# Kernel optimization log

Hardware: AMD Instinct MI355X
Metric: run time of the kernel (lower is better)

The kernel has to match this reference:

```python
import jax, jax.numpy as jnp
import numpy as np

SPLINE_ORDER = 3
BN_EPS = 1e-5


def make_grid(grid_size, lo=-1.0, hi=1.0):
    # torch KANLinear grid: uniform on [lo,hi] extended by spline_order knots each side
    h = (hi - lo) / grid_size
    return jnp.arange(-SPLINE_ORDER, grid_size + SPLINE_ORDER + 1, dtype=jnp.float32) * h + lo


def b_splines(x, grid, k=SPLINE_ORDER):
    # x: [...], grid: [G+2k+1] -> bases [..., G+k] (Cox-de Boor recursion)
    x = x[..., None]
    bases = ((x >= grid[:-1]) & (x < grid[1:])).astype(x.dtype)
    for j in range(1, k + 1):
        left = (x - grid[: -(j + 1)]) / (grid[j:-1] - grid[: -(j + 1)])
        right = (grid[j + 1:] - x) / (grid[j + 1:] - grid[1:-j])
        bases = left * bases[..., :-1] + right * bases[..., 1:]
    return bases


def extract_patches(x, d):
    # 3x3 dilated sliding windows, stride 1, padding == dilation -> same HxW
    B, C, H, W = x.shape
    xp = jnp.pad(x, ((0, 0), (0, 0), (d, d), (d, d)))
    pats = [xp[:, :, ki * d:ki * d + H, kj * d:kj * d + W]
            for ki in range(3) for kj in range(3)]
    return jnp.stack(pats, axis=-1)  # [B,C,H,W,9] (kh-major, matching torch Unfold)


def batchnorm(x, g, b):
    # training-mode BN (torch default forward): batch statistics, biased variance
    mean = x.mean(axis=(0, 2, 3), keepdims=True)
    var = x.var(axis=(0, 2, 3), keepdims=True)
    return (x - mean) / jnp.sqrt(var + BN_EPS) * g[None, :, None, None] + b[None, :, None, None]


def se_block(x, w1, w2):
    y = x.mean(axis=(2, 3))                                  # [B,C]
    y = jax.nn.sigmoid(jax.nn.relu(y @ w1.T) @ w2.T)         # [B,C]
    return x * y[:, :, None, None]


def kan_conv(x, base_w, spline_w, grid, dilation):
    # one KANLinear(9->1) per (out,in) channel pair, summed over in channels
    p = extract_patches(x, dilation)                          # [B,Ci,H,W,9]
    base = jnp.einsum('bihwk,oik->bohw', jax.nn.silu(p), base_w)
    bs = b_splines(p, grid)                                   # [B,Ci,H,W,9,G+k]
    spl = jnp.einsum('bihwkg,oikg->bohw', bs, spline_w)
    return base + spl


def kan_branch(x, base_w, spline_w, grid, dilation, bn_g, bn_b, se_w1, se_w2):
    y = kan_conv(x, base_w, spline_w, grid, dilation)
    y = jax.nn.relu(batchnorm(y, bn_g, bn_b))
    return se_block(y, se_w1, se_w2)


def setup_inputs() -> dict:
    key = jax.random.key(0)
    ks = jax.random.split(key, 16)
    B, Ci, Co, H, W = 2, 64, 64, 64, 64
    r = Co // 16
    d = {"x": jax.random.normal(ks[0], (B, Ci, H, W), jnp.float32)}
    for i, (bname, G) in enumerate([(6, 3), (12, 6), (18, 9)]):
        kk = jax.random.split(ks[1 + i], 4)
        d[f"base_w{bname}"] = jax.random.normal(kk[0], (Co, Ci, 9), jnp.float32) / np.sqrt(9.0 * Ci)
        d[f"spline_w{bname}"] = jax.random.normal(kk[1], (Co, Ci, 9, G + SPLINE_ORDER), jnp.float32) * (0.1 / np.sqrt(9.0 * Ci))
        d[f"bn{bname}_g"] = jnp.ones((Co,), jnp.float32)
        d[f"bn{bname}_b"] = jnp.zeros((Co,), jnp.float32)
        d[f"se{bname}_w1"] = jax.random.normal(kk[2], (r, Co), jnp.float32) / np.sqrt(Co)
        d[f"se{bname}_w2"] = jax.random.normal(kk[3], (Co, r), jnp.float32) / np.sqrt(r)
    d["gp_conv_w"] = jax.random.normal(ks[4], (Co, Ci), jnp.float32) / np.sqrt(Ci)
    d["gp_conv_b"] = jnp.zeros((Co,), jnp.float32)
    d["gp_bn_g"] = jnp.ones((Co,), jnp.float32)
    d["gp_bn_b"] = jnp.zeros((Co,), jnp.float32)
    d["gp_se_w1"] = jax.random.normal(ks[5], (r, Co), jnp.float32) / np.sqrt(Co)
    d["gp_se_w2"] = jax.random.normal(ks[6], (Co, r), jnp.float32) / np.sqrt(r)
    d["fuse_w"] = jax.random.normal(ks[7], (Co, 4 * Co), jnp.float32) / np.sqrt(4.0 * Co)
    d["fuse_b"] = jnp.zeros((Co,), jnp.float32)
    d["fuse_bn_g"] = jnp.ones((Co,), jnp.float32)
    d["fuse_bn_b"] = jnp.zeros((Co,), jnp.float32)
    return d


def reference(x, base_w6, spline_w6, bn6_g, bn6_b, se6_w1, se6_w2,
              base_w12, spline_w12, bn12_g, bn12_b, se12_w1, se12_w2,
              base_w18, spline_w18, bn18_g, bn18_b, se18_w1, se18_w2,
              gp_conv_w, gp_conv_b, gp_bn_g, gp_bn_b, gp_se_w1, gp_se_w2,
              fuse_w, fuse_b, fuse_bn_g, fuse_bn_b):
    B, Ci, H, W = x.shape
    # global-pool branch: avgpool -> 1x1 conv -> BN -> ReLU -> SE -> bilinear
    # upsample (1x1 source => pure broadcast, align_corners irrelevant)
    gp = x.mean(axis=(2, 3)) @ gp_conv_w.T + gp_conv_b      # [B,Co]
    gp = gp[:, :, None, None]
    gp = jax.nn.relu(batchnorm(gp, gp_bn_g, gp_bn_b))
    gp = se_block(gp, gp_se_w1, gp_se_w2)
    gp = jnp.broadcast_to(gp, (B, gp.shape[1], H, W))
    # KAN dilated branches
    b6 = kan_branch(x, base_w6, spline_w6, make_grid(3), 6, bn6_g, bn6_b, se6_w1, se6_w2)
    b12 = kan_branch(x, base_w12, spline_w12, make_grid(6), 12, bn12_g, bn12_b, se12_w1, se12_w2)
    b18 = kan_branch(x, base_w18, spline_w18, make_grid(9), 18, bn18_g, bn18_b, se18_w1, se18_w2)
    cat = jnp.concatenate([b6, b12, b18, gp], axis=1)        # [B,4Co,H,W]
    out = jnp.einsum('bihw,oi->bohw', cat, fuse_w) + fuse_b[None, :, None, None]
    out = jax.nn.relu(batchnorm(out, fuse_bn_g, fuse_bn_b))
    return out
```

## Files before the change

kernel.cpp:

```cpp
#include <hip/hip_runtime.h>
#include <hip/hip_bf16.h>
#include <math.h>

#define DEV __device__ __forceinline__

static constexpr int HW  = 4096;
static constexpr int POS = 8192;
static constexpr int SLAB = 6 * 64 * 4096;

typedef __attribute__((ext_vector_type(8)))  short short8;
typedef __attribute__((ext_vector_type(16))) float floatx16;

template<int G>
DEV void bsplines(float x, float* out ) {
  const float h = 2.0f / (float)G;
  float knot[G + 7];
#pragma unroll
  for (int t = 0; t < G + 7; ++t) knot[t] = -1.0f + (float)(t - 3) * h;
  float bb[G + 6];
#pragma unroll
  for (int t = 0; t < G + 6; ++t) bb[t] = (x >= knot[t] && x < knot[t + 1]) ? 1.0f : 0.0f;
#pragma unroll
  for (int j = 1; j <= 3; ++j) {
    const float inv = (float)G / (2.0f * (float)j);
#pragma unroll
    for (int t = 0; t < G + 6 - j; ++t) {
      float left  = (x - knot[t]) * inv;
      float right = (knot[t + j + 1] - x) * inv;
      bb[t] = left * bb[t] + right * bb[t + 1];
    }
  }
#pragma unroll
  for (int t = 0; t < G + 3; ++t) out[t] = bb[t];
}

DEV float sigmoidf_(float x) { return 1.0f / (1.0f + __expf(-x)); }

DEV float block_reduce_256(float v, float* sb) {
  __syncthreads();
#pragma unroll
  for (int off = 32; off > 0; off >>= 1) v += __shfl_down(v, off, 64);
  int lane = threadIdx.x & 63, wid = threadIdx.x >> 6;
  if (lane == 0) sb[wid] = v;
  __syncthreads();
  return sb[0] + sb[1] + sb[2] + sb[3];
}


template<int CF>
DEV void wprep_body(const float* __restrict__ base_w, const float* __restrict__ spline_w,
                    __hip_bfloat16* __restrict__ Wt, int bid) {
  constexpr int KC = 64 * CF;
  int lin = bid * 256 + threadIdx.x;
  int ic = lin % KC;
  int rest = lin / KC;
  int o = rest & 63, tap = rest >> 6;
  int c = ic % CF, i = ic / CF;
  float v = (c == 0) ? base_w[(o * 64 + i) * 9 + tap]
                     : spline_w[((o * 64 + i) * 9 + tap) * (CF - 1) + (c - 1)];
  Wt[lin] = __float2bfloat16(v);
}

template<int G>
DEV void c0r_body(int ki, const float* __restrict__ sw, float* __restrict__ out,
                  float* shmem ) {
  constexpr int NB = G + 3;
  int o = threadIdx.x & 63, part = threadIdx.x >> 6;
  float b0[NB];
  bsplines<G>(0.0f, b0);
  float s = 0.0f;
  for (int kj = 0; kj < 3; ++kj) {
    int tap = ki * 3 + kj;
    for (int i = part * 16; i < part * 16 + 16; ++i) {
      const float* p = sw + ((size_t)(o * 64 + i) * 9 + tap) * NB;
#pragma unroll
      for (int c = 0; c < NB; ++c) s += p[c] * b0[c];
    }
  }
  shmem[part * 64 + o] = s;
  __syncthreads();
  if (part == 0)
    out[ki * 64 + o] = shmem[o] + shmem[64 + o] + shmem[128 + o] + shmem[192 + o];
}

__global__ void prep_k(const float* bw0, const float* sw0, const float* bw1, const float* sw1,
                       const float* bw2, const float* sw2,
                       __hip_bfloat16* W0, __hip_bfloat16* W1, __hip_bfloat16* W2,
                       float* C0r, const float* fuse_w, float* fwT,
                       const float* x, float* xm, float* accz ) {
  __shared__ float shmem[256];
  int bid = blockIdx.x, tid = threadIdx.x;
  if (bid < 1008)      { wprep_body<7>(bw0, sw0, W0, bid); }
  else if (bid < 2448) { wprep_body<10>(bw1, sw1, W1, bid - 1008); }
  else if (bid < 4320) { wprep_body<13>(bw2, sw2, W2, bid - 2448); }
  else if (bid < 4329) {
    int idx = bid - 4320, br = idx / 3, ki = idx % 3;
    if (br == 0)      c0r_body<3>(ki, sw0, C0r, shmem);
    else if (br == 1) c0r_body<6>(ki, sw1, C0r + 192, shmem);
    else              c0r_body<9>(ki, sw2, C0r + 384, shmem);
  } else if (bid < 4377) {
    int lin = (bid - 4329) * 256 + tid;
    int o = lin & 63, i2 = lin >> 6;
    fwT[i2 * 64 + o] = fuse_w[o * 256 + i2];
  } else if (bid < 4505) {
    int bi = bid - 4377;
    const float* p = x + (size_t)bi * HW;
    float s = 0.0f;
    for (int t = tid; t < HW; t += 256) s += p[t];
    s = block_reduce_256(s, shmem);
    if (tid == 0) xm[bi] = s * (1.0f / HW);
  } else {
    for (int t = tid; t < 896; t += 256) accz[t] = 0.0f;
  }
}

template<int G, int D>
DEV void features_body(const float* __restrict__ x, __hip_bfloat16* __restrict__ F, int bid,
                       __hip_bfloat16* lds ) {
  constexpr int CF = G + 4;
  constexpr int NB = G + 3;
  constexpr int WP = 64 + 2 * D;
  constexpr int NG = WP / 4;
  constexpr int KC = 64 * CF;
  int i = threadIdx.x & 63, ws = threadIdx.x >> 6;
  int wpg = bid % NG;
  int rest = bid / NG;
  int h = rest & 63, b = rest >> 6;
  int wp = wpg * 4 + ws;
  int w = wp - D;
  float xv = (w >= 0 && w < 64) ? x[((size_t)(b * 64 + i) * 64 + h) * 64 + w] : 0.0f;
  float s = xv * sigmoidf_(xv);
  float bas[NB];
  bsplines<G>(xv, bas);
  __hip_bfloat16* dst = lds + (ws * 64 + i) * CF;
  dst[0] = __float2bfloat16(s);
#pragma unroll
  for (int c = 1; c < CF; ++c) dst[c] = __float2bfloat16(bas[c - 1]);
  __syncthreads();
  constexpr int TOT2 = 4 * 64 * CF / 2;
  uint* g = (uint*)(F + ((size_t)((b * 64 + h) * WP) + wpg * 4) * KC);
  const uint* l = (const uint*)lds;
  for (int t = threadIdx.x; t < TOT2; t += 256) g[t] = l[t];
}

__global__ void features_all_k(const float* __restrict__ x, __hip_bfloat16* F0,
                               __hip_bfloat16* F1, __hip_bfloat16* F2) {
  __shared__ __hip_bfloat16 lds[4 * 64 * 13];
  int bid = blockIdx.x;
  if (bid < 2432)      features_body<3, 6>(x, F0, bid, lds);
  else if (bid < 5248) features_body<6, 12>(x, F1, bid - 2432, lds);
  else                 features_body<9, 18>(x, F2, bid - 5248, lds);
}

DEV floatx16 mfma_bf16(short8 a, short8 b, floatx16 c) {
  return __builtin_amdgcn_mfma_f32_32x32x16_bf16(a, b, c, 0, 0, 0);
}

template<int CF, int DD>
DEV void conv_dev(int ki, int b, int hp, const short* __restrict__ F,
                  const short* __restrict__ W, const float* __restrict__ C0r,
                  float* __restrict__ ypart, int br) {
  constexpr int KC = 64 * CF;
  constexpr int WP = 64 + 2 * DD;
  int wv = threadIdx.x >> 6;
  int lane = threadIdx.x & 63;
  int lr = lane & 31, lq = lane >> 5;
  int hs = hp * 2 + wv;
  int h_out = hs - (ki - 1) * DD;
  bool valid = (h_out >= 0 && h_out < 64);
  int h_tgt = valid ? h_out : (h_out < 0 ? h_out + 64 : h_out - 64);
  float* yb = ypart + (size_t)ki * SLAB + ((size_t)((br * 2 + b) * 64 + h_tgt)) * 4096;

  if (!valid) {
    const float* c0 = C0r + (br * 3 + ki) * 64;
#pragma unroll
    for (int wh = 0; wh < 2; ++wh) {
      int w = wh * 32 + lr;
#pragma unroll
      for (int ot = 0; ot < 2; ++ot)
#pragma unroll
        for (int reg = 0; reg < 16; ++reg) {
          int o = (reg & 3) + 8 * (reg >> 2) + 4 * lq + 32 * ot;
          yb[(size_t)o * 64 + w] = c0[o];
        }
    }
    return;
  }

  floatx16 acc[2][2];
#pragma unroll
  for (int ot = 0; ot < 2; ++ot)
#pragma unroll
    for (int wh = 0; wh < 2; ++wh)
#pragma unroll
      for (int r = 0; r < 16; ++r) acc[ot][wh][r] = 0.0f;

  const short* rowF = F + (size_t)(b * 64 + hs) * WP * KC;
  const short* wb = W + (size_t)(ki * 3) * 64 * KC + lr * KC + lq * 8;
  const short* fb = rowF + lr * KC + lq * 8;
#pragma unroll
  for (int kj = 0; kj < 3; ++kj) {
    const short* w0p = wb + kj * (64 * KC);
    const short* f0p = fb + kj * (DD * KC);
#pragma unroll 4
    for (int s = 0; s < 4 * CF; ++s) {
      short8 a0 = *(const short8*)(w0p + s * 16);
      short8 a1 = *(const short8*)(w0p + 32 * KC + s * 16);
      short8 b0 = *(const short8*)(f0p + s * 16);
      short8 b1 = *(const short8*)(f0p + 32 * KC + s * 16);
      acc[0][0] = mfma_bf16(a0, b0, acc[0][0]);
      acc[0][1] = mfma_bf16(a0, b1, acc[0][1]);
      acc[1][0] = mfma_bf16(a1, b0, acc[1][0]);
      acc[1][1] = mfma_bf16(a1, b1, acc[1][1]);
    }
  }

#pragma unroll
  for (int ot = 0; ot < 2; ++ot)
#pragma unroll
    for (int wh = 0; wh < 2; ++wh) {
      int w = wh * 32 + lr;
#pragma unroll
      for (int reg = 0; reg < 16; ++reg) {
        int o = (reg & 3) + 8 * (reg >> 2) + 4 * lq + 32 * ot;
        yb[(size_t)o * 64 + w] = acc[ot][wh][reg];
      }
    }
}

__global__ __launch_bounds__(128) void conv_all_k(
    const short* __restrict__ F0, const short* __restrict__ F1, const short* __restrict__ F2,
    const short* __restrict__ W0, const short* __restrict__ W1, const short* __restrict__ W2,
    const float* __restrict__ C0r, float* __restrict__ ypart) {
  int bid = blockIdx.x;
  int e  = bid & 7;
  int t  = bid >> 3;
  int ki = t % 3;
  int m  = (t / 3) * 8 + e;
  int br = m >> 6, b = (m >> 5) & 1, hp = m & 31;
  if (br == 0)      conv_dev<7, 6>(ki, b, hp, F0, W0, C0r, ypart, 0);
  else if (br == 1) conv_dev<10, 12>(ki, b, hp, F1, W1, C0r, ypart, 1);
  else              conv_dev<13, 18>(ki, b, hp, F2, W2, C0r, ypart, 2);
}

__global__ void rb_k(float* __restrict__ yp, float* __restrict__ bnacc_s,
                     float* __restrict__ bnacc_q) {
  int bid = blockIdx.x;
  int bb = bid / 256, chunk = bid % 256;
  int br = bb >> 1;
  int tid = threadIdx.x;
  size_t base = (size_t)bb * 262144 + chunk * 1024 + tid * 4;
  float4 v = *(const float4*)(yp + base);
#pragma unroll
  for (int s2 = 1; s2 < 3; ++s2) {
    float4 u = *(const float4*)(yp + base + (size_t)s2 * SLAB);
    v.x += u.x; v.y += u.y; v.z += u.z; v.w += u.w;
  }
  *(float4*)(yp + base) = v;
  float s = v.x + v.y + v.z + v.w;
  float q = v.x * v.x + v.y * v.y + v.z * v.z + v.w * v.w;
  s += __shfl_down(s, 8, 16); s += __shfl_down(s, 4, 16);
  s += __shfl_down(s, 2, 16); s += __shfl_down(s, 1, 16);
  q += __shfl_down(q, 8, 16); q += __shfl_down(q, 4, 16);
  q += __shfl_down(q, 2, 16); q += __shfl_down(q, 1, 16);
  if ((tid & 15) == 0) {
    int o = (chunk * 16 + (tid >> 4)) & 63;
    atomicAdd(&bnacc_s[br * 64 + o], s);
    atomicAdd(&bnacc_q[br * 64 + o], q);
  }
}

__global__ void sesum_k(const float* __restrict__ y, const float* __restrict__ bnacc_s,
                        const float* __restrict__ bnacc_q,
                        const float* g0, const float* b0p, const float* g1, const float* b1p,
                        const float* g2, const float* b2p, float* __restrict__ se_acc) {
  int bid = blockIdx.x;
  int bb = bid >> 6, h = bid & 63;
  int br = bb >> 1;
  int tid = threadIdx.x;
  int o = tid >> 2, wq = tid & 3;
  const float* gptr = (br == 0) ? g0 : ((br == 1) ? g1 : g2);
  const float* bptr = (br == 0) ? b0p : ((br == 1) ? b1p : b2p);
  float mu = bnacc_s[br * 64 + o] * (1.0f / POS);
  float var = bnacc_q[br * 64 + o] * (1.0f / POS) - mu * mu;
  float kk = gptr[o] / sqrtf(var + 1e-5f);
  float cc = bptr[o] - mu * kk;
  const float* row = y + (size_t)bb * 262144 + (size_t)h * 4096 + o * 64 + wq * 16;
  float s = 0.0f;
#pragma unroll
  for (int j = 0; j < 4; ++j) {
    float4 v = *(const float4*)(row + j * 4);
    float a;
    a = v.x * kk + cc; s += (a > 0.0f) ? a : 0.0f;
    a = v.y * kk + cc; s += (a > 0.0f) ? a : 0.0f;
    a = v.z * kk + cc; s += (a > 0.0f) ? a : 0.0f;
    a = v.w * kk + cc; s += (a > 0.0f) ? a : 0.0f;
  }
  s += __shfl_down(s, 2, 4);
  s += __shfl_down(s, 1, 4);
  if (wq == 0) atomicAdd(&se_acc[bb * 64 + o], s);
}

__global__ void semlp_gp_k(const float* __restrict__ se_acc,
                           const float* __restrict__ bnacc_s, const float* __restrict__ bnacc_q,
                           const float* g0, const float* b0p, const float* g1, const float* b1p,
                           const float* g2, const float* b2p,
                           const float* w10, const float* w11, const float* w12,
                           const float* w20, const float* w21, const float* w22,
                           float* __restrict__ A1, float* __restrict__ A0,
                           const float* __restrict__ xm, const float* __restrict__ gw,
                           const float* __restrict__ gb, const float* __restrict__ bng,
                           const float* __restrict__ bnb, const float* __restrict__ gpw1,
                           const float* __restrict__ gpw2, const float* __restrict__ fuse_w,
                           float* __restrict__ fuse_gp) {
  __shared__ float sm[64];
  __shared__ float g0s[2][64], gp1s[2][64], gpvs[2][64];
  int tid = threadIdx.x;
  if (blockIdx.x < 6) {
    int bb = blockIdx.x, br = bb >> 1;
    const float* w1 = (br == 0) ? w10 : ((br == 1) ? w11 : w12);
    const float* w2 = (br == 0) ? w20 : ((br == 1) ? w21 : w22);
    const float* gptr = (br == 0) ? g0 : ((br == 1) ? g1 : g2);
    const float* bptr = (br == 0) ? b0p : ((br == 1) ? b1p : b2p);
    if (tid < 64) sm[tid] = se_acc[bb * 64 + tid] * (1.0f / HW);
    __syncthreads();
    if (tid < 64) {
      int o = tid;
      float z[4];
#pragma unroll
      for (int j = 0; j < 4; ++j) {
        float s = 0.0f;
        for (int c2 = 0; c2 < 64; ++c2) s += sm[c2] * w1[j * 64 + c2];
        z[j] = (s > 0.0f) ? s : 0.0f;
      }
      float t = 0.0f;
#pragma unroll
      for (int j = 0; j < 4; ++j) t += z[j] * w2[o * 4 + j];
      t = sigmoidf_(t);
      float mu = bnacc_s[br * 64 + o] * (1.0f / POS);
      float var = bnacc_q[br * 64 + o] * (1.0f / POS) - mu * mu;
      float kk = gptr[o] / sqrtf(var + 1e-5f);
      float cc = bptr[o] - mu * kk;
      A1[bb * 64 + o] = kk * t;
      A0[bb * 64 + o] = cc * t;
    }
  } else {
    int b = tid >> 6, o = tid & 63;
    float gv = gb[o];
    for (int i = 0; i < 64; ++i) gv += xm[b * 64 + i] * gw[o * 64 + i];
    g0s[b][o] = gv;
    __syncthreads();
    float mu = 0.5f * (g0s[0][o] + g0s[1][o]);
    float df = g0s[0][o] - g0s[1][o];
    float var = 0.25f * df * df;
    float v = (gv - mu) / sqrtf(var + 1e-5f) * bng[o] + bnb[o];
    v = (v > 0.0f) ? v : 0.0f;
    gp1s[b][o] = v;
    __syncthreads();
    float z[4];
#pragma unroll
    for (int j = 0; j < 4; ++j) {
      float s = 0.0f;
      for (int c2 = 0; c2 < 64; ++c2) s += gp1s[b][c2] * gpw1[j * 64 + c2];
      z[j] = (s > 0.0f) ? s : 0.0f;
    }
    float t = 0.0f;
#pragma unroll
    for (int j = 0; j < 4; ++j) t += z[j] * gpw2[o * 4 + j];
    t = sigmoidf_(t);
    gpvs[b][o] = v * t;
    __syncthreads();
    float fg = 0.0f;
    for (int c2 = 0; c2 < 64; ++c2) fg += fuse_w[o * 256 + 192 + c2] * gpvs[b][c2];
    fuse_gp[b * 64 + o] = fg;
  }
}

__global__ __launch_bounds__(256) void fuse_k(
    const float* __restrict__ y, const float* __restrict__ A1, const float* __restrict__ A0,
    const float* __restrict__ fwT, const float* __restrict__ fb, const float* __restrict__ fgp,
    float* __restrict__ tmp, float* __restrict__ fstat) {
  int bid = blockIdx.x;
  int b = bid >> 7, h = (bid >> 1) & 63, wh = bid & 1;
  int tid = threadIdx.x;
  int wg = tid & 7, og = tid >> 3;
  int w0 = wg * 4, o0 = og * 2;
  float acc[2][4] = {};
  __shared__ float As[64][32];
  __shared__ float Ws[64][64];
  for (int br = 0; br < 3; ++br) {
#pragma unroll
    for (int m = 0; m < 8; ++m) {
      int lin = tid + m * 256;
      int oc = lin >> 5, wl = lin & 31;
      float v = y[(size_t)(br * 2 + b) * 262144 + (size_t)h * 4096 + oc * 64 + wh * 32 + wl];
      float a1 = A1[(br * 2 + b) * 64 + oc], a0 = A0[(br * 2 + b) * 64 + oc];
      v = v * a1 + a0;
      As[oc][wl] = (v > 0.0f) ? v : 0.0f;
    }
#pragma unroll
    for (int m = 0; m < 16; ++m) {
      int lin = tid + m * 256;
      int oc = lin >> 6, ol = lin & 63;
      Ws[oc][ol] = fwT[(br * 64 + oc) * 64 + ol];
    }
    __syncthreads();
#pragma unroll 8
    for (int ict = 0; ict < 64; ++ict) {
      float4 a = *reinterpret_cast<const float4*>(&As[ict][w0]);
      float2 wv = *reinterpret_cast<const float2*>(&Ws[ict][o0]);
      acc[0][0] += wv.x * a.x; acc[0][1] += wv.x * a.y; acc[0][2] += wv.x * a.z; acc[0][3] += wv.x * a.w;
      acc[1][0] += wv.y * a.x; acc[1][1] += wv.y * a.y; acc[1][2] += wv.y * a.z; acc[1][3] += wv.y * a.w;
    }
    __syncthreads();
  }
  float* tp = tmp + (size_t)(b * 64 + h) * 4096 + wh * 32;
  float ps[2], pq[2];
#pragma unroll
  for (int oo = 0; oo < 2; ++oo) {
    int o = o0 + oo;
    float bias = fb[o] + fgp[b * 64 + o];
    float4 v = make_float4(acc[oo][0] + bias, acc[oo][1] + bias,
                           acc[oo][2] + bias, acc[oo][3] + bias);
    *reinterpret_cast<float4*>(&tp[o * 64 + w0]) = v;
    ps[oo] = v.x + v.y + v.z + v.w;
    pq[oo] = v.x * v.x + v.y * v.y + v.z * v.z + v.w * v.w;
  }
  __syncthreads();
#pragma unroll
  for (int oo = 0; oo < 2; ++oo) { As[o0 + oo][wg] = ps[oo]; Ws[o0 + oo][wg] = pq[oo]; }
  __syncthreads();
  if (tid < 64) {
    float s = 0.0f, q = 0.0f;
#pragma unroll
    for (int r = 0; r < 8; ++r) { s += As[tid][r]; q += Ws[tid][r]; }
    atomicAdd(&fstat[tid], s);
    atomicAdd(&fstat[64 + tid], q);
  }
}

__global__ void final_k(const float* __restrict__ tmp, const float* __restrict__ fstat,
                        const float* __restrict__ g, const float* __restrict__ bb,
                        float* __restrict__ out) {
  int lin = blockIdx.x * 256 + threadIdx.x;
  int w = lin & 63, h2 = (lin >> 6) & 63, o = (lin >> 12) & 63, b = lin >> 18;
  float v = tmp[((size_t)(b * 64 + h2) * 64 + o) * 64 + w];
  float m = fstat[o] * (1.0f / POS);
  float var = fstat[64 + o] * (1.0f / POS) - m * m;
  float kk = g[o] / sqrtf(var + 1e-5f);
  float r = (v - m) * kk + bb[o];
  out[lin] = (r > 0.0f) ? r : 0.0f;
}

extern "C" void kernel_launch(void* const* d_in, const int* in_sizes, int n_in,
                              void* d_out, int out_size, void* d_ws, size_t ws_size,
                              hipStream_t stream) {
  const float* x = (const float*)d_in[0];
  const float* base_w[3]   = {(const float*)d_in[1],  (const float*)d_in[7],  (const float*)d_in[13]};
  const float* spline_w[3] = {(const float*)d_in[2],  (const float*)d_in[8],  (const float*)d_in[14]};
  const float* bn_g[3]     = {(const float*)d_in[3],  (const float*)d_in[9],  (const float*)d_in[15]};
  const float* bn_b[3]     = {(const float*)d_in[4],  (const float*)d_in[10], (const float*)d_in[16]};
  const float* se_w1[3]    = {(const float*)d_in[5],  (const float*)d_in[11], (const float*)d_in[17]};
  const float* se_w2[3]    = {(const float*)d_in[6],  (const float*)d_in[12], (const float*)d_in[18]};
  const float* gp_conv_w = (const float*)d_in[19];
  const float* gp_conv_b = (const float*)d_in[20];
  const float* gp_bn_g   = (const float*)d_in[21];
  const float* gp_bn_b   = (const float*)d_in[22];
  const float* gp_se_w1  = (const float*)d_in[23];
  const float* gp_se_w2  = (const float*)d_in[24];
  const float* fuse_w    = (const float*)d_in[25];
  const float* fuse_b    = (const float*)d_in[26];
  const float* fuse_bn_g = (const float*)d_in[27];
  const float* fuse_bn_b = (const float*)d_in[28];
  float* out = (float*)d_out;

  char* wsp = (char*)d_ws;
  auto alloc = [&](size_t bytes) -> char* {
    char* p = wsp;
    wsp += (bytes + 255) & ~(size_t)255;
    return p;
  };
  __hip_bfloat16* F0 = (__hip_bfloat16*)alloc((size_t)2 * 64 * 76 * 448 * 2);
  __hip_bfloat16* F1 = (__hip_bfloat16*)alloc((size_t)2 * 64 * 88 * 640 * 2);
  __hip_bfloat16* F2 = (__hip_bfloat16*)alloc((size_t)2 * 64 * 100 * 832 * 2);
  __hip_bfloat16* W0 = (__hip_bfloat16*)alloc((size_t)9 * 64 * 448 * 2);
  __hip_bfloat16* W1 = (__hip_bfloat16*)alloc((size_t)9 * 64 * 640 * 2);
  __hip_bfloat16* W2 = (__hip_bfloat16*)alloc((size_t)9 * 64 * 832 * 2);
  float* C0r   = (float*)alloc((size_t)3 * 3 * 64 * 4);
  float* ypart = (float*)alloc((size_t)3 * SLAB * 4);
  float* y     = ypart;
  float* tmp   = ypart + SLAB;
  float* A1  = (float*)alloc(384 * 4);
  float* A0  = (float*)alloc(384 * 4);
  float* xm  = (float*)alloc(128 * 4);
  float* fgp = (float*)alloc(128 * 4);
  float* fwT = (float*)alloc((size_t)12288 * 4);
  float* accz = (float*)alloc(896 * 4);
  float* fstat   = accz;
  float* bnacc_s = accz + 128;
  float* bnacc_q = accz + 320;
  float* se_acc  = accz + 512;

  prep_k<<<4506, 256, 0, stream>>>(base_w[0], spline_w[0], base_w[1], spline_w[1],
                                   base_w[2], spline_w[2], W0, W1, W2, C0r,
                                   fuse_w, fwT, x, xm, accz);
  features_all_k<<<8448, 256, 0, stream>>>(x, F0, F1, F2);
  conv_all_k<<<576, 128, 0, stream>>>(
      (const short*)F0, (const short*)F1, (const short*)F2,
      (const short*)W0, (const short*)W1, (const short*)W2, C0r, ypart);
  rb_k<<<1536, 256, 0, stream>>>(ypart, bnacc_s, bnacc_q);
  sesum_k<<<384, 256, 0, stream>>>(y, bnacc_s, bnacc_q, bn_g[0], bn_b[0], bn_g[1], bn_b[1],
                                   bn_g[2], bn_b[2], se_acc);
  semlp_gp_k<<<7, 128, 0, stream>>>(se_acc, bnacc_s, bnacc_q, bn_g[0], bn_b[0], bn_g[1], bn_b[1],
                                    bn_g[2], bn_b[2], se_w1[0], se_w1[1], se_w1[2],
                                    se_w2[0], se_w2[1], se_w2[2], A1, A0,
                                    xm, gp_conv_w, gp_conv_b, gp_bn_g, gp_bn_b,
                                    gp_se_w1, gp_se_w2, fuse_w, fgp);
  fuse_k<<<256, 256, 0, stream>>>(y, A1, A0, fwT, fuse_b, fgp, tmp, fstat);
  final_k<<<2048, 256, 0, stream>>>(tmp, fstat, fuse_bn_g, fuse_bn_b, out);
}
```

Before: 296.3 us.

## Merge prep with features, fuse BN/SE reductions, and fold SE MLP into fuse kernel

Combines the weight-prep and feature-expansion kernels into one launch, replaces the separate split-K reduce, BN-stat, and SE-sum kernels with a single per-channel kernel that sums the partials and computes both statistics without atomics, and recomputes the SE MLP and global-pool branch redundantly inside every fuse block. The aim is to cut launch count and inter-kernel gaps. In exchange, the new reduction kernel runs only 192 blocks, each striding through memory at 256-byte steps with poor coalescing. Every fuse block also repeats a small serial MLP.

```diff
diff --git a/kernel.cpp b/kernel.cpp
--- a/kernel.cpp
+++ b/kernel.cpp
@@ -81,37 +81,6 @@
   __syncthreads();
   if (part == 0)
     out[ki * 64 + o] = shmem[o] + shmem[64 + o] + shmem[128 + o] + shmem[192 + o];
-}
-
-__global__ void prep_k(const float* bw0, const float* sw0, const float* bw1, const float* sw1,
-                       const float* bw2, const float* sw2,
-                       __hip_bfloat16* W0, __hip_bfloat16* W1, __hip_bfloat16* W2,
-                       float* C0r, const float* fuse_w, float* fwT,
-                       const float* x, float* xm, float* accz ) {
-  __shared__ float shmem[256];
-  int bid = blockIdx.x, tid = threadIdx.x;
-  if (bid < 1008)      { wprep_body<7>(bw0, sw0, W0, bid); }
-  else if (bid < 2448) { wprep_body<10>(bw1, sw1, W1, bid - 1008); }
-  else if (bid < 4320) { wprep_body<13>(bw2, sw2, W2, bid - 2448); }
-  else if (bid < 4329) {
-    int idx = bid - 4320, br = idx / 3, ki = idx % 3;
-    if (br == 0)      c0r_body<3>(ki, sw0, C0r, shmem);
-    else if (br == 1) c0r_body<6>(ki, sw1, C0r + 192, shmem);
-    else              c0r_body<9>(ki, sw2, C0r + 384, shmem);
-  } else if (bid < 4377) {
-    int lin = (bid - 4329) * 256 + tid;
-    int o = lin & 63, i2 = lin >> 6;
-    fwT[i2 * 64 + o] = fuse_w[o * 256 + i2];
-  } else if (bid < 4505) {
-    int bi = bid - 4377;
-    const float* p = x + (size_t)bi * HW;
-    float s = 0.0f;
-    for (int t = tid; t < HW; t += 256) s += p[t];
-    s = block_reduce_256(s, shmem);
-    if (tid == 0) xm[bi] = s * (1.0f / HW);
-  } else {
-    for (int t = tid; t < 896; t += 256) accz[t] = 0.0f;
-  }
 }
 
 template<int G, int D>
@@ -143,13 +112,42 @@
   for (int t = threadIdx.x; t < TOT2; t += 256) g[t] = l[t];
 }
 
-__global__ void features_all_k(const float* __restrict__ x, __hip_bfloat16* F0,
-                               __hip_bfloat16* F1, __hip_bfloat16* F2) {
+__global__ void prepfeat_k(const float* __restrict__ x,
+                           __hip_bfloat16* F0, __hip_bfloat16* F1, __hip_bfloat16* F2,
+                           const float* bw0, const float* sw0, const float* bw1,
+                           const float* sw1, const float* bw2, const float* sw2,
+                           __hip_bfloat16* W0, __hip_bfloat16* W1, __hip_bfloat16* W2,
+                           float* C0r, const float* fuse_w, float* fwT,
+                           float* xm, float* accz ) {
   __shared__ __hip_bfloat16 lds[4 * 64 * 13];
-  int bid = blockIdx.x;
-  if (bid < 2432)      features_body<3, 6>(x, F0, bid, lds);
-  else if (bid < 5248) features_body<6, 12>(x, F1, bid - 2432, lds);
-  else                 features_body<9, 18>(x, F2, bid - 5248, lds);
+  __shared__ float shmem[256];
+  int bid = blockIdx.x, tid = threadIdx.x;
+  if (bid < 2432)      { features_body<3, 6>(x, F0, bid, lds); return; }
+  else if (bid < 5248) { features_body<6, 12>(x, F1, bid - 2432, lds); return; }
+  else if (bid < 8448) { features_body<9, 18>(x, F2, bid - 5248, lds); return; }
+  int pb = bid - 8448;
+  if (pb < 1008)      { wprep_body<7>(bw0, sw0, W0, pb); }
+  else if (pb < 2448) { wprep_body<10>(bw1, sw1, W1, pb - 1008); }
+  else if (pb < 4320) { wprep_body<13>(bw2, sw2, W2, pb - 2448); }
+  else if (pb < 4329) {
+    int idx = pb - 4320, br = idx / 3, ki = idx % 3;
+    if (br == 0)      c0r_body<3>(ki, sw0, C0r, shmem);
+    else if (br == 1) c0r_body<6>(ki, sw1, C0r + 192, shmem);
+    else              c0r_body<9>(ki, sw2, C0r + 384, shmem);
+  } else if (pb < 4377) {
+    int lin = (pb - 4329) * 256 + tid;
+    int o = lin & 63, i2 = lin >> 6;
+    fwT[i2 * 64 + o] = fuse_w[o * 256 + i2];
+  } else if (pb < 4505) {
+    int bi = pb - 4377;
+    const float* p = x + (size_t)bi * HW;
+    float s = 0.0f;
+    for (int t = tid; t < HW; t += 256) s += p[t];
+    s = block_reduce_256(s, shmem);
+    if (tid == 0) xm[bi] = s * (1.0f / HW);
+  } else {
+    for (int t = tid; t < 896; t += 256) accz[t] = 0.0f;
+  }
 }
 
 DEV floatx16 mfma_bf16(short8 a, short8 b, floatx16 c) {
@@ -243,94 +241,88 @@
   else              conv_dev<13, 18>(ki, b, hp, F2, W2, C0r, ypart, 2);
 }
 
-__global__ void rb_k(float* __restrict__ yp, float* __restrict__ bnacc_s,
-                     float* __restrict__ bnacc_q) {
-  int bid = blockIdx.x;
-  int bb = bid / 256, chunk = bid % 256;
-  int br = bb >> 1;
-  int tid = threadIdx.x;
-  size_t base = (size_t)bb * 262144 + chunk * 1024 + tid * 4;
-  float4 v = *(const float4*)(yp + base);
-#pragma unroll
-  for (int s2 = 1; s2 < 3; ++s2) {
-    float4 u = *(const float4*)(yp + base + (size_t)s2 * SLAB);
-    v.x += u.x; v.y += u.y; v.z += u.z; v.w += u.w;
-  }
-  *(float4*)(yp + base) = v;
-  float s = v.x + v.y + v.z + v.w;
-  float q = v.x * v.x + v.y * v.y + v.z * v.z + v.w * v.w;
-  s += __shfl_down(s, 8, 16); s += __shfl_down(s, 4, 16);
-  s += __shfl_down(s, 2, 16); s += __shfl_down(s, 1, 16);
-  q += __shfl_down(q, 8, 16); q += __shfl_down(q, 4, 16);
-  q += __shfl_down(q, 2, 16); q += __shfl_down(q, 1, 16);
-  if ((tid & 15) == 0) {
-    int o = (chunk * 16 + (tid >> 4)) & 63;
-    atomicAdd(&bnacc_s[br * 64 + o], s);
-    atomicAdd(&bnacc_q[br * 64 + o], q);
-  }
-}
-
-__global__ void sesum_k(const float* __restrict__ y, const float* __restrict__ bnacc_s,
-                        const float* __restrict__ bnacc_q,
-                        const float* g0, const float* b0p, const float* g1, const float* b1p,
-                        const float* g2, const float* b2p, float* __restrict__ se_acc) {
-  int bid = blockIdx.x;
-  int bb = bid >> 6, h = bid & 63;
-  int br = bb >> 1;
-  int tid = threadIdx.x;
-  int o = tid >> 2, wq = tid & 3;
+__global__ void bnsesum_k(float* __restrict__ yp, float* __restrict__ bnacc_s,
+                          float* __restrict__ bnacc_q,
+                          const float* g0, const float* b0p, const float* g1, const float* b1p,
+                          const float* g2, const float* b2p, float* __restrict__ se_acc) {
+  int br = blockIdx.x >> 6, o = blockIdx.x & 63;
+  __shared__ float sb[4];
+  float s = 0.0f, q = 0.0f;
+  for (int idx = threadIdx.x; idx < POS; idx += 256) {
+    int b = idx >> 12, rem = idx & 4095;
+    int h = rem >> 6, w = rem & 63;
+    size_t base = ((size_t)((br * 2 + b) * 64 + h)) * 4096 + o * 64 + w;
+    float v = yp[base] + yp[base + SLAB] + yp[base + 2 * (size_t)SLAB];
+    yp[base] = v;
+    s += v; q += v * v;
+  }
+  s = block_reduce_256(s, sb);
+  q = block_reduce_256(q, sb);
+  if (threadIdx.x == 0) { bnacc_s[br * 64 + o] = s; bnacc_q[br * 64 + o] = q; }
+  float m = s * (1.0f / POS);
+  float var = q * (1.0f / POS) - m * m;
   const float* gptr = (br == 0) ? g0 : ((br == 1) ? g1 : g2);
   const float* bptr = (br == 0) ? b0p : ((br == 1) ? b1p : b2p);
-  float mu = bnacc_s[br * 64 + o] * (1.0f / POS);
-  float var = bnacc_q[br * 64 + o] * (1.0f / POS) - mu * mu;
   float kk = gptr[o] / sqrtf(var + 1e-5f);
-  float cc = bptr[o] - mu * kk;
-  const float* row = y + (size_t)bb * 262144 + (size_t)h * 4096 + o * 64 + wq * 16;
-  float s = 0.0f;
-#pragma unroll
-  for (int j = 0; j < 4; ++j) {
-    float4 v = *(const float4*)(row + j * 4);
-    float a;
-    a = v.x * kk + cc; s += (a > 0.0f) ? a : 0.0f;
-    a = v.y * kk + cc; s += (a > 0.0f) ? a : 0.0f;
-    a = v.z * kk + cc; s += (a > 0.0f) ? a : 0.0f;
-    a = v.w * kk + cc; s += (a > 0.0f) ? a : 0.0f;
-  }
-  s += __shfl_down(s, 2, 4);
-  s += __shfl_down(s, 1, 4);
-  if (wq == 0) atomicAdd(&se_acc[bb * 64 + o], s);
-}
-
-__global__ void semlp_gp_k(const float* __restrict__ se_acc,
-                           const float* __restrict__ bnacc_s, const float* __restrict__ bnacc_q,
-                           const float* g0, const float* b0p, const float* g1, const float* b1p,
-                           const float* g2, const float* b2p,
-                           const float* w10, const float* w11, const float* w12,
-                           const float* w20, const float* w21, const float* w22,
-                           float* __restrict__ A1, float* __restrict__ A0,
-                           const float* __restrict__ xm, const float* __restrict__ gw,
-                           const float* __restrict__ gb, const float* __restrict__ bng,
-                           const float* __restrict__ bnb, const float* __restrict__ gpw1,
-                           const float* __restrict__ gpw2, const float* __restrict__ fuse_w,
-                           float* __restrict__ fuse_gp) {
-  __shared__ float sm[64];
-  __shared__ float g0s[2][64], gp1s[2][64], gpvs[2][64];
+  float cc = bptr[o] - m * kk;
+  float s0 = 0.0f, s1 = 0.0f;
+  for (int idx = threadIdx.x; idx < POS; idx += 256) {
+    int b = idx >> 12, rem = idx & 4095;
+    int h = rem >> 6, w = rem & 63;
+    float a = yp[((size_t)((br * 2 + b) * 64 + h)) * 4096 + o * 64 + w] * kk + cc;
+    a = (a > 0.0f) ? a : 0.0f;
+    if (b == 0) s0 += a; else s1 += a;
+  }
+  s0 = block_reduce_256(s0, sb);
+  s1 = block_reduce_256(s1, sb);
+  if (threadIdx.x == 0) {
+    se_acc[(br * 2 + 0) * 64 + o] = s0;
+    se_acc[(br * 2 + 1) * 64 + o] = s1;
+  }
+}
+
+__global__ __launch_bounds__(256) void fuse_k(
+    const float* __restrict__ y, const float* __restrict__ se_acc,
+    const float* __restrict__ bnacc_s, const float* __restrict__ bnacc_q,
+    const float* g0, const float* b0p, const float* g1, const float* b1p,
+    const float* g2, const float* b2p,
+    const float* w10, const float* w11, const float* w12,
+    const float* w20, const float* w21, const float* w22,
+    const float* __restrict__ xm, const float* __restrict__ gw,
+    const float* __restrict__ gb, const float* __restrict__ bng,
+    const float* __restrict__ bnb, const float* __restrict__ gpw1,
+    const float* __restrict__ gpw2, const float* __restrict__ fuse_w,
+    const float* __restrict__ fwT, const float* __restrict__ fb,
+    float* __restrict__ tmp, float* __restrict__ fstat) {
+  __shared__ float As[64][32];
+  __shared__ float Ws[64][64];
+  __shared__ float sem[384], A1l[384], A0l[384], fgpl[128], gsc[384];
+  int bid = blockIdx.x;
+  int b = bid >> 7, h = (bid >> 1) & 63, wh = bid & 1;
   int tid = threadIdx.x;
-  if (blockIdx.x < 6) {
-    int bb = blockIdx.x, br = bb >> 1;
-    const float* w1 = (br == 0) ? w10 : ((br == 1) ? w11 : w12);
-    const float* w2 = (br == 0) ? w20 : ((br == 1) ? w21 : w22);
-    const float* gptr = (br == 0) ? g0 : ((br == 1) ? g1 : g2);
-    const float* bptr = (br == 0) ? b0p : ((br == 1) ? b1p : b2p);
-    if (tid < 64) sm[tid] = se_acc[bb * 64 + tid] * (1.0f / HW);
-    __syncthreads();
-    if (tid < 64) {
-      int o = tid;
+
+  for (int u = tid; u < 384; u += 256) sem[u] = se_acc[u] * (1.0f / HW);
+  __syncthreads();
+  if (tid < 128) {
+    int bgp = tid >> 6, o = tid & 63;
+    float gv = gb[o];
+    for (int i = 0; i < 64; ++i) gv += xm[bgp * 64 + i] * gw[o * 64 + i];
+    gsc[tid] = gv;
+  }
+  if (tid < 64) {
+    int o = tid;
+#pragma unroll
+    for (int bb = 0; bb < 6; ++bb) {
+      int br = bb >> 1;
+      const float* w1 = (br == 0) ? w10 : ((br == 1) ? w11 : w12);
+      const float* w2 = (br == 0) ? w20 : ((br == 1) ? w21 : w22);
+      const float* g_ = (br == 0) ? g0 : ((br == 1) ? g1 : g2);
+      const float* b_ = (br == 0) ? b0p : ((br == 1) ? b1p : b2p);
       float z[4];
 #pragma unroll
       for (int j = 0; j < 4; ++j) {
         float s = 0.0f;
-        for (int c2 = 0; c2 < 64; ++c2) s += sm[c2] * w1[j * 64 + c2];
+        for (int c2 = 0; c2 < 64; ++c2) s += sem[bb * 64 + c2] * w1[j * 64 + c2];
         z[j] = (s > 0.0f) ? s : 0.0f;
       }
       float t = 0.0f;
@@ -339,63 +331,57 @@
       t = sigmoidf_(t);
       float mu = bnacc_s[br * 64 + o] * (1.0f / POS);
       float var = bnacc_q[br * 64 + o] * (1.0f / POS) - mu * mu;
-      float kk = gptr[o] / sqrtf(var + 1e-5f);
-      float cc = bptr[o] - mu * kk;
-      A1[bb * 64 + o] = kk * t;
-      A0[bb * 64 + o] = cc * t;
-    }
-  } else {
-    int b = tid >> 6, o = tid & 63;
-    float gv = gb[o];
-    for (int i = 0; i < 64; ++i) gv += xm[b * 64 + i] * gw[o * 64 + i];
-    g0s[b][o] = gv;
-    __syncthreads();
-    float mu = 0.5f * (g0s[0][o] + g0s[1][o]);
-    float df = g0s[0][o] - g0s[1][o];
+      float kk = g_[o] / sqrtf(var + 1e-5f);
+      float cc = b_[o] - mu * kk;
+      A1l[bb * 64 + o] = kk * t;
+      A0l[bb * 64 + o] = cc * t;
+    }
+  }
+  __syncthreads();
+  if (tid < 128) {
+    int o = tid & 63;
+    float mu = 0.5f * (gsc[o] + gsc[64 + o]);
+    float df = gsc[o] - gsc[64 + o];
     float var = 0.25f * df * df;
-    float v = (gv - mu) / sqrtf(var + 1e-5f) * bng[o] + bnb[o];
-    v = (v > 0.0f) ? v : 0.0f;
-    gp1s[b][o] = v;
-    __syncthreads();
+    float v = (gsc[tid] - mu) / sqrtf(var + 1e-5f) * bng[o] + bnb[o];
+    gsc[128 + tid] = (v > 0.0f) ? v : 0.0f;
+  }
+  __syncthreads();
+  if (tid < 128) {
+    int bgp = tid >> 6, o = tid & 63;
     float z[4];
 #pragma unroll
     for (int j = 0; j < 4; ++j) {
       float s = 0.0f;
-      for (int c2 = 0; c2 < 64; ++c2) s += gp1s[b][c2] * gpw1[j * 64 + c2];
+      for (int c2 = 0; c2 < 64; ++c2) s += gsc[128 + bgp * 64 + c2] * gpw1[j * 64 + c2];
       z[j] = (s > 0.0f) ? s : 0.0f;
     }
     float t = 0.0f;
 #pragma unroll
     for (int j = 0; j < 4; ++j) t += z[j] * gpw2[o * 4 + j];
     t = sigmoidf_(t);
-    gpvs[b][o] = v * t;
-    __syncthreads();
+    gsc[256 + tid] = gsc[128 + tid] * t;
+  }
+  __syncthreads();
+  if (tid < 128) {
+    int bgp = tid >> 6, o = tid & 63;
     float fg = 0.0f;
-    for (int c2 = 0; c2 < 64; ++c2) fg += fuse_w[o * 256 + 192 + c2] * gpvs[b][c2];
-    fuse_gp[b * 64 + o] = fg;
-  }
-}
-
-__global__ __launch_bounds__(256) void fuse_k(
-    const float* __restrict__ y, const float* __restrict__ A1, const float* __restrict__ A0,
-    const float* __restrict__ fwT, const float* __restrict__ fb, const float* __restrict__ fgp,
-    float* __restrict__ tmp, float* __restrict__ fstat) {
-  int bid = blockIdx.x;
-  int b = bid >> 7, h = (bid >> 1) & 63, wh = bid & 1;
-  int tid = threadIdx.x;
+    for (int c2 = 0; c2 < 64; ++c2) fg += fuse_w[o * 256 + 192 + c2] * gsc[256 + bgp * 64 + c2];
+    fgpl[tid] = fg;
+  }
+  __syncthreads();
+
   int wg = tid & 7, og = tid >> 3;
   int w0 = wg * 4, o0 = og * 2;
   float acc[2][4] = {};
-  __shared__ float As[64][32];
-  __shared__ float Ws[64][64];
   for (int br = 0; br < 3; ++br) {
 #pragma unroll
     for (int m = 0; m < 8; ++m) {
       int lin = tid + m * 256;
       int oc = lin >> 5, wl = lin & 31;
       float v = y[(size_t)(br * 2 + b) * 262144 + (size_t)h * 4096 + oc * 64 + wh * 32 + wl];
-      float a1 = A1[(br * 2 + b) * 64 + oc], a0 = A0[(br * 2 + b) * 64 + oc];
-      v = v * a1 + a0;
+      int idx = (br * 2 + b) * 64 + oc;
+      v = v * A1l[idx] + A0l[idx];
       As[oc][wl] = (v > 0.0f) ? v : 0.0f;
     }
 #pragma unroll
@@ -419,7 +405,7 @@
 #pragma unroll
   for (int oo = 0; oo < 2; ++oo) {
     int o = o0 + oo;
-    float bias = fb[o] + fgp[b * 64 + o];
+    float bias = fb[o] + fgpl[b * 64 + o];
     float4 v = make_float4(acc[oo][0] + bias, acc[oo][1] + bias,
                            acc[oo][2] + bias, acc[oo][3] + bias);
     *reinterpret_cast<float4*>(&tp[o * 64 + w0]) = v;
@@ -490,10 +476,7 @@
   float* ypart = (float*)alloc((size_t)3 * SLAB * 4);
   float* y     = ypart;
   float* tmp   = ypart + SLAB;
-  float* A1  = (float*)alloc(384 * 4);
-  float* A0  = (float*)alloc(384 * 4);
   float* xm  = (float*)alloc(128 * 4);
-  float* fgp = (float*)alloc(128 * 4);
   float* fwT = (float*)alloc((size_t)12288 * 4);
   float* accz = (float*)alloc(896 * 4);
   float* fstat   = accz;
@@ -501,21 +484,19 @@
   float* bnacc_q = accz + 320;
   float* se_acc  = accz + 512;
 
-  prep_k<<<4506, 256, 0, stream>>>(base_w[0], spline_w[0], base_w[1], spline_w[1],
-                                   base_w[2], spline_w[2], W0, W1, W2, C0r,
-                                   fuse_w, fwT, x, xm, accz);
-  features_all_k<<<8448, 256, 0, stream>>>(x, F0, F1, F2);
+  prepfeat_k<<<12954, 256, 0, stream>>>(x, F0, F1, F2,
+                                        base_w[0], spline_w[0], base_w[1], spline_w[1],
+                                        base_w[2], spline_w[2], W0, W1, W2, C0r,
+                                        fuse_w, fwT, xm, accz);
   conv_all_k<<<576, 128, 0, stream>>>(
       (const short*)F0, (const short*)F1, (const short*)F2,
       (const short*)W0, (const short*)W1, (const short*)W2, C0r, ypart);
-  rb_k<<<1536, 256, 0, stream>>>(ypart, bnacc_s, bnacc_q);
-  sesum_k<<<384, 256, 0, stream>>>(y, bnacc_s, bnacc_q, bn_g[0], bn_b[0], bn_g[1], bn_b[1],
-                                   bn_g[2], bn_b[2], se_acc);
-  semlp_gp_k<<<7, 128, 0, stream>>>(se_acc, bnacc_s, bnacc_q, bn_g[0], bn_b[0], bn_g[1], bn_b[1],
-                                    bn_g[2], bn_b[2], se_w1[0], se_w1[1], se_w1[2],
-                                    se_w2[0], se_w2[1], se_w2[2], A1, A0,
-                                    xm, gp_conv_w, gp_conv_b, gp_bn_g, gp_bn_b,
-                                    gp_se_w1, gp_se_w2, fuse_w, fgp);
-  fuse_k<<<256, 256, 0, stream>>>(y, A1, A0, fwT, fuse_b, fgp, tmp, fstat);
+  bnsesum_k<<<192, 256, 0, stream>>>(ypart, bnacc_s, bnacc_q, bn_g[0], bn_b[0],
+                                     bn_g[1], bn_b[1], bn_g[2], bn_b[2], se_acc);
+  fuse_k<<<256, 256, 0, stream>>>(y, se_acc, bnacc_s, bnacc_q,
+                                  bn_g[0], bn_b[0], bn_g[1], bn_b[1], bn_g[2], bn_b[2],
+                                  se_w1[0], se_w1[1], se_w1[2], se_w2[0], se_w2[1], se_w2[2],
+                                  xm, gp_conv_w, gp_conv_b, gp_bn_g, gp_bn_b,
+                                  gp_se_w1, gp_se_w2, fuse_w, fwT, fuse_b, tmp, fstat);
   final_k<<<2048, 256, 0, stream>>>(tmp, fstat, fuse_bn_g, fuse_bn_b, out);
 }
```

Measured after the change: 302.4 us. 2.1% more time.
